# Performance work log

Measured on AMD Instinct MI355X. Metric: run time of the kernel, lower is better.

## Reference

```python
import jax, jax.numpy as jnp
import numpy as np

B, M, P, A, T = 32, 128, 20, 32, 32
H = 32   # embed_size / local hidden
E = 64   # local_hidden_dim = 2*H, global attention embed dim


def setup_inputs() -> dict:
    key = jax.random.key(0)
    ks = jax.random.split(key, 10)
    def w(k, shape, fan):
        return jax.random.normal(k, shape, jnp.float32) / np.float32(np.sqrt(fan))
    z = lambda *s: jnp.zeros(s, jnp.float32)
    o = lambda *s: jnp.ones(s, jnp.float32)
    return {
        "map_states": jax.random.normal(ks[0], (B, M, P, 16), jnp.float32),
        "agent_states": jax.random.normal(ks[1], (B, A, T, 4), jnp.float32),
        "m_W1": w(ks[2], (16, H), 16), "m_b1": z(H), "m_g1": o(H), "m_be1": z(H),
        "m_W2": w(ks[3], (H, H), H),   "m_b2": z(H), "m_g2": o(H), "m_be2": z(H),
        "a_W1": w(ks[4], (4, H), 4),   "a_b1": z(H), "a_g1": o(H), "a_be1": z(H),
        "a_W2": w(ks[5], (H, H), H),   "a_b2": z(H), "a_g2": o(H), "a_be2": z(H),
        # stacked attention params: index 0 = a2m, 1 = agent(self), 2 = m2a
        "att_Wq": w(ks[6], (3, E, E), E), "att_bq": z(3, E),
        "att_Wk": w(ks[7], (3, E, E), E), "att_bk": z(3, E),
        "att_Wv": w(ks[8], (3, E, E), E), "att_bv": z(3, E),
        "att_Wo": w(ks[9], (3, E, E), E), "att_bo": z(3, E),
    }


def _mlp(x, W, b, g, be):
    # Linear -> LayerNorm -> ReLU
    h = x @ W + b
    mu = jnp.mean(h, axis=-1, keepdims=True)
    var = jnp.var(h, axis=-1, keepdims=True)
    h = (h - mu) / jnp.sqrt(var + 1e-5) * g + be
    return jax.nn.relu(h)


def _local_graph(x, p1, p2):
    # x: [B, N, P, F] -> [B, N, 2H]
    e = _mlp(_mlp(x, *p1), *p2)                       # [B,N,P,H]
    n = e.shape[2]
    # faithful "max excluding self": max_j (e[j] - 10000*[j==i])
    mask = -10000.0 * jnp.eye(n, dtype=e.dtype)       # [Pi,Pj]
    nb = jnp.max(e[:, :, None, :, :] + mask[None, None, :, :, None], axis=3)  # [B,N,P,H]
    e = jnp.concatenate([e, nb], axis=-1)             # [B,N,P,2H]
    return jnp.max(e, axis=2)                          # [B,N,2H]


def _mha(q, k, v, Wq, bq, Wk, bk, Wv, bv, Wo, bo):
    # single-head attention, batch_first
    d = q.shape[-1]
    Q = q @ Wq + bq
    K = k @ Wk + bk
    V = v @ Wv + bv
    scores = jnp.einsum('bqd,bkd->bqk', Q, K) / jnp.sqrt(jnp.asarray(d, Q.dtype))
    attn = jax.nn.softmax(scores, axis=-1)
    return jnp.einsum('bqk,bkd->bqd', attn, V) @ Wo + bo


def reference(map_states, agent_states,
              m_W1, m_b1, m_g1, m_be1, m_W2, m_b2, m_g2, m_be2,
              a_W1, a_b1, a_g1, a_be1, a_W2, a_b2, a_g2, a_be2,
              att_Wq, att_bq, att_Wk, att_bk, att_Wv, att_bv, att_Wo, att_bo):
    map_emb = _local_graph(map_states, (m_W1, m_b1, m_g1, m_be1), (m_W2, m_b2, m_g2, m_be2))      # [B,M,E]
    agent_emb = _local_graph(agent_states, (a_W1, a_b1, a_g1, a_be1), (a_W2, a_b2, a_g2, a_be2))  # [B,A,E]

    target = agent_emb[:, :1]                                       # [B,1,E]
    kv = jnp.concatenate([target, map_emb], axis=1)                 # [B,M+1,E]
    a2m = _mha(map_emb, kv, kv, att_Wq[0], att_bq[0], att_Wk[0], att_bk[0],
               att_Wv[0], att_bv[0], att_Wo[0], att_bo[0])
    map_emb = map_emb + a2m
    t_a = _mha(target, target, target, att_Wq[1], att_bq[1], att_Wk[1], att_bk[1],
               att_Wv[1], att_bv[1], att_Wo[1], att_bo[1])
    t_m2a = _mha(target, map_emb, map_emb, att_Wq[2], att_bq[2], att_Wk[2], att_bk[2],
                 att_Wv[2], att_bv[2], att_Wo[2], att_bo[2])
    target = t_a + t_m2a                                            # [B,1,E]
    # pack (target_agent_embedding, map_embedding) into one array [B, M+1, E]
    return jnp.concatenate([target, map_emb], axis=1)
```

## Files before the change

### kernel.cpp

```cpp
#include <hip/hip_runtime.h>

#define BB 32
#define MM 128
#define PP 20
#define AA 32
#define TT 32
#define HH 32
#define EE 64

__device__ __forceinline__ float4 matvec64(const float* __restrict__ W,
                                           const float* __restrict__ xrow,
                                           int s, int t)
{
    const float4* __restrict__ Wv = (const float4*)W;
    const float4* __restrict__ xv = (const float4*)xrow;
    float4 acc = make_float4(0.f, 0.f, 0.f, 0.f);
#pragma unroll
    for (int ii = 0; ii < 4; ++ii) {
        const float4 xx = xv[s * 4 + ii];
        const int ib = s * 16 + ii * 4;
        const float4 w0 = Wv[(ib + 0) * 16 + t];
        const float4 w1 = Wv[(ib + 1) * 16 + t];
        const float4 w2 = Wv[(ib + 2) * 16 + t];
        const float4 w3 = Wv[(ib + 3) * 16 + t];
        acc.x = fmaf(xx.x, w0.x, acc.x); acc.y = fmaf(xx.x, w0.y, acc.y);
        acc.z = fmaf(xx.x, w0.z, acc.z); acc.w = fmaf(xx.x, w0.w, acc.w);
        acc.x = fmaf(xx.y, w1.x, acc.x); acc.y = fmaf(xx.y, w1.y, acc.y);
        acc.z = fmaf(xx.y, w1.z, acc.z); acc.w = fmaf(xx.y, w1.w, acc.w);
        acc.x = fmaf(xx.z, w2.x, acc.x); acc.y = fmaf(xx.z, w2.y, acc.y);
        acc.z = fmaf(xx.z, w2.z, acc.z); acc.w = fmaf(xx.z, w2.w, acc.w);
        acc.x = fmaf(xx.w, w3.x, acc.x); acc.y = fmaf(xx.w, w3.y, acc.y);
        acc.z = fmaf(xx.w, w3.z, acc.z); acc.w = fmaf(xx.w, w3.w, acc.w);
    }
    acc.x += __shfl_xor(acc.x, 16); acc.y += __shfl_xor(acc.y, 16);
    acc.z += __shfl_xor(acc.z, 16); acc.w += __shfl_xor(acc.w, 16);
    acc.x += __shfl_xor(acc.x, 32); acc.y += __shfl_xor(acc.y, 32);
    acc.z += __shfl_xor(acc.z, 32); acc.w += __shfl_xor(acc.w, 32);
    return acc;
}

template <int IN>
__device__ __forceinline__ void lg_qkv_body(const float* __restrict__ xg, int P,
                                            const float* __restrict__ W1, const float* __restrict__ b1,
                                            const float* __restrict__ g1, const float* __restrict__ be1,
                                            const float* __restrict__ W2, const float* __restrict__ b2,
                                            const float* __restrict__ g2, const float* __restrict__ be2,
                                            float* __restrict__ embRow,
                                            const float* __restrict__ Wq, const float* __restrict__ bq,
                                            const float* __restrict__ Wk, const float* __restrict__ bk,
                                            const float* __restrict__ Wv, const float* __restrict__ bv,
                                            float* __restrict__ Qrow,
                                            float* __restrict__ Krow,
                                            float* __restrict__ Vrow)
{
    const int tid  = threadIdx.x;
    const int wave = tid >> 6;
    const int lane = tid & 63;
    const int sub  = tid >> 5;
    const int c    = tid & 31;

    __shared__ __align__(16) float aslot[4][32];
    __shared__ __align__(16) float wmax[2][32];
    __shared__ __align__(16) float xrow[EE];

    float w1c[IN];
#pragma unroll
    for (int k = 0; k < IN; ++k) w1c[k] = W1[k * HH + c];
    float w2c[HH];
#pragma unroll
    for (int k = 0; k < HH; ++k) w2c[k] = W2[k * HH + c];
    const float b1c = b1[c], g1c = g1[c], be1c = be1[c];
    const float b2c = b2[c], g2c = g2[c], be2c = be2[c];

    float cmax = -1e30f;

    for (int p0 = 0; p0 < P; p0 += 4) {
        const int p = p0 + sub;
        const float* xp = xg + (long)p * IN;

        float h = b1c;
        if (IN == 16) {
            const float4* xp4 = (const float4*)xp;
            const float4 x0 = xp4[0], x1 = xp4[1], x2 = xp4[2], x3 = xp4[3];
            h = fmaf(x0.x, w1c[0], h);  h = fmaf(x0.y, w1c[1], h);
            h = fmaf(x0.z, w1c[2], h);  h = fmaf(x0.w, w1c[3], h);
            h = fmaf(x1.x, w1c[4], h);  h = fmaf(x1.y, w1c[5], h);
            h = fmaf(x1.z, w1c[6], h);  h = fmaf(x1.w, w1c[7], h);
            h = fmaf(x2.x, w1c[8], h);  h = fmaf(x2.y, w1c[9], h);
            h = fmaf(x2.z, w1c[10], h); h = fmaf(x2.w, w1c[11], h);
            h = fmaf(x3.x, w1c[12], h); h = fmaf(x3.y, w1c[13], h);
            h = fmaf(x3.z, w1c[14], h); h = fmaf(x3.w, w1c[15], h);
        } else {
            const float4 x0 = *(const float4*)xp;
            h = fmaf(x0.x, w1c[0], h); h = fmaf(x0.y, w1c[1], h);
            h = fmaf(x0.z, w1c[2], h); h = fmaf(x0.w, w1c[3], h);
        }

        float sdot = h;
#pragma unroll
        for (int off = 16; off >= 1; off >>= 1) sdot += __shfl_xor(sdot, off, 32);
        const float mu = sdot * (1.0f / 32.0f);
        float d = h - mu;
        float sq = d * d;
#pragma unroll
        for (int off = 16; off >= 1; off >>= 1) sq += __shfl_xor(sq, off, 32);
        const float var = sq * (1.0f / 32.0f);
        float a = d * rsqrtf(var + 1e-5f) * g1c + be1c;
        a = fmaxf(a, 0.0f);

        aslot[sub][c] = a;
        const float4* av4 = (const float4*)aslot[sub];
        float h2 = b2c;
#pragma unroll
        for (int j = 0; j < 8; ++j) {
            const float4 aa = av4[j];
            h2 = fmaf(aa.x, w2c[4 * j + 0], h2);
            h2 = fmaf(aa.y, w2c[4 * j + 1], h2);
            h2 = fmaf(aa.z, w2c[4 * j + 2], h2);
            h2 = fmaf(aa.w, w2c[4 * j + 3], h2);
        }

        float s2 = h2;
#pragma unroll
        for (int off = 16; off >= 1; off >>= 1) s2 += __shfl_xor(s2, off, 32);
        const float mu2 = s2 * (1.0f / 32.0f);
        float d2 = h2 - mu2;
        float sq2 = d2 * d2;
#pragma unroll
        for (int off = 16; off >= 1; off >>= 1) sq2 += __shfl_xor(sq2, off, 32);
        const float var2 = sq2 * (1.0f / 32.0f);
        float e = d2 * rsqrtf(var2 + 1e-5f) * g2c + be2c;
        e = fmaxf(e, 0.0f);

        cmax = fmaxf(cmax, e);
    }

    cmax = fmaxf(cmax, __shfl_xor(cmax, 32));
    if (lane < 32) wmax[wave][lane] = cmax;
    __syncthreads();

    if (tid < 32) {
        const float fin = fmaxf(wmax[0][tid], wmax[1][tid]);
        xrow[tid]      = fin;
        xrow[tid + 32] = fin;
        embRow[tid]      = fin;
        embRow[tid + 32] = fin;
    }
    __syncthreads();

    const int s = lane >> 4, t = lane & 15;
    if (wave == 0) {
        if (Qrow) {
            float4 q4 = matvec64(Wq, xrow, s, t);
            if (s == 0) {
                const float4 bq4 = ((const float4*)bq)[t];
                float4 qo;
                qo.x = (q4.x + bq4.x) * 0.125f;
                qo.y = (q4.y + bq4.y) * 0.125f;
                qo.z = (q4.z + bq4.z) * 0.125f;
                qo.w = (q4.w + bq4.w) * 0.125f;
                ((float4*)Qrow)[t] = qo;
            }
        }
        float4 k4 = matvec64(Wk, xrow, s, t);
        if (s == 0) {
            const float4 kb4 = ((const float4*)bk)[t];
            float4 ko;
            ko.x = k4.x + kb4.x; ko.y = k4.y + kb4.y;
            ko.z = k4.z + kb4.z; ko.w = k4.w + kb4.w;
            ((float4*)Krow)[t] = ko;
        }
    } else {
        float4 v4 = matvec64(Wv, xrow, s, t);
        if (s == 0) {
            const float4 vb4 = ((const float4*)bv)[t];
            float4 vo;
            vo.x = v4.x + vb4.x; vo.y = v4.y + vb4.y;
            vo.z = v4.z + vb4.z; vo.w = v4.w + vb4.w;
            ((float4*)Vrow)[t] = vo;
        }
    }
}

__global__ void lg_qkv_kernel(const float* __restrict__ map_states,
                              const float* __restrict__ agent_states,
                              const float* __restrict__ mW1, const float* __restrict__ mb1,
                              const float* __restrict__ mg1, const float* __restrict__ mbe1,
                              const float* __restrict__ mW2, const float* __restrict__ mb2,
                              const float* __restrict__ mg2, const float* __restrict__ mbe2,
                              const float* __restrict__ aW1, const float* __restrict__ ab1,
                              const float* __restrict__ ag1, const float* __restrict__ abe1,
                              const float* __restrict__ aW2, const float* __restrict__ ab2,
                              const float* __restrict__ ag2, const float* __restrict__ abe2,
                              const float* __restrict__ Wq, const float* __restrict__ bq,
                              const float* __restrict__ Wk, const float* __restrict__ bk,
                              const float* __restrict__ Wv, const float* __restrict__ bv,
                              float* __restrict__ map_emb,
                              float* __restrict__ target,
                              float* __restrict__ Qb,
                              float* __restrict__ Kb,
                              float* __restrict__ Vb)
{
    const int g = blockIdx.x;
    if (g < BB * MM) {
        const int b = g >> 7, m = g & 127;
        lg_qkv_body<16>(map_states + (long)g * PP * 16, PP,
                        mW1, mb1, mg1, mbe1, mW2, mb2, mg2, mbe2,
                        map_emb + (long)g * EE,
                        Wq, bq, Wk, bk, Wv, bv,
                        Qb + (long)g * EE,
                        Kb + ((long)b * 129 + 1 + m) * EE,
                        Vb + ((long)b * 129 + 1 + m) * EE);
    } else {
        const int b = g - BB * MM;
        lg_qkv_body<4>(agent_states + (long)b * AA * TT * 4, TT,
                       aW1, ab1, ag1, abe1, aW2, ab2, ag2, abe2,
                       target + (long)b * EE,
                       Wq, bq, Wk, bk, Wv, bv,
                       nullptr,
                       Kb + (long)b * 129 * EE,
                       Vb + (long)b * 129 * EE);
    }
}

__global__ void attn_fused_kernel(const float* __restrict__ map_emb,
                                  const float* __restrict__ Qb,
                                  const float* __restrict__ Kb,
                                  const float* __restrict__ Vb,
                                  const float* __restrict__ Wo, const float* __restrict__ bo,
                                  const float* __restrict__ Wk2, const float* __restrict__ bk2,
                                  const float* __restrict__ Wv2, const float* __restrict__ bv2,
                                  float* __restrict__ K2,
                                  float* __restrict__ V2,
                                  float* __restrict__ out)
{
    const int blk  = blockIdx.x;
    const int b    = blk >> 7;
    const int q    = blk & 127;
    const int lane = threadIdx.x;
    const int s = lane >> 4, t = lane & 15;

    __shared__ __align__(16) float sc[132];
    __shared__ __align__(16) float av[EE];
    __shared__ __align__(16) float resrow[EE];

    const float4 q4 = ((const float4*)(Qb + ((long)b * MM + q) * EE))[t];

    const float* Kbase = Kb + (long)b * 129 * EE;
    float mx = -1e30f;
#pragma unroll 4
    for (int it = 0; it < 33; ++it) {
        const int j = it * 4 + s;
        const bool valid = (j < 129);
        float p = 0.0f;
        if (valid) {
            const float4 k4 = ((const float4*)(Kbase + (long)j * EE))[t];
            p = q4.x * k4.x + q4.y * k4.y + q4.z * k4.z + q4.w * k4.w;
        }
        p += __shfl_xor(p, 1); p += __shfl_xor(p, 2);
        p += __shfl_xor(p, 4); p += __shfl_xor(p, 8);
        if (valid) {
            mx = fmaxf(mx, p);
            if (t == 0) sc[j] = p;
        }
    }
#pragma unroll
    for (int off = 32; off >= 1; off >>= 1) mx = fmaxf(mx, __shfl_xor(mx, off));
    __syncthreads();

    float sum = 0.0f;
    for (int j = lane; j < 129; j += 64) {
        const float e = __expf(sc[j] - mx);
        sc[j] = e;
        sum += e;
    }
#pragma unroll
    for (int off = 32; off >= 1; off >>= 1) sum += __shfl_xor(sum, off);
    const float inv = 1.0f / sum;
    __syncthreads();

    const float* Vbase = Vb + (long)b * 129 * EE;
    float a0 = 0.f, a1 = 0.f, a2 = 0.f, a3 = 0.f;
#pragma unroll 4
    for (int j0 = 0; j0 < 128; j0 += 4) {
        const float4 s4 = *(const float4*)&sc[j0];
        a0 = fmaf(s4.x, Vbase[(long)(j0 + 0) * EE + lane], a0);
        a1 = fmaf(s4.y, Vbase[(long)(j0 + 1) * EE + lane], a1);
        a2 = fmaf(s4.z, Vbase[(long)(j0 + 2) * EE + lane], a2);
        a3 = fmaf(s4.w, Vbase[(long)(j0 + 3) * EE + lane], a3);
    }
    a0 = fmaf(sc[128], Vbase[(long)128 * EE + lane], a0);
    const float acc = ((a0 + a1) + (a2 + a3)) * inv;
    av[lane] = acc;
    __syncthreads();

    const float4 o4 = matvec64(Wo, av, s, t);
    const float4 bo4 = ((const float4*)bo)[t];
    const float4 x4 = ((const float4*)(map_emb + ((long)b * MM + q) * EE))[t];
    float4 res;
    res.x = o4.x + bo4.x + x4.x;
    res.y = o4.y + bo4.y + x4.y;
    res.z = o4.z + bo4.z + x4.z;
    res.w = o4.w + bo4.w + x4.w;
    if (s == 0) {
        ((float4*)(out + ((long)b * 129 + 1 + q) * EE))[t] = res;
        ((float4*)resrow)[t] = res;
    }
    __syncthreads();

    const float4 k4 = matvec64(Wk2, resrow, s, t);
    const float4 v4 = matvec64(Wv2, resrow, s, t);
    if (s == 0) {
        const float4 kb4 = ((const float4*)bk2)[t];
        const float4 vb4 = ((const float4*)bv2)[t];
        float4 ko, vo;
        ko.x = k4.x + kb4.x; ko.y = k4.y + kb4.y; ko.z = k4.z + kb4.z; ko.w = k4.w + kb4.w;
        vo.x = v4.x + vb4.x; vo.y = v4.y + vb4.y; vo.z = v4.z + vb4.z; vo.w = v4.w + vb4.w;
        ((float4*)(K2 + ((long)b * MM + q) * EE))[t] = ko;
        ((float4*)(V2 + ((long)b * MM + q) * EE))[t] = vo;
    }
}

__global__ void target_kernel(const float* __restrict__ target,
                              const float* __restrict__ K2, const float* __restrict__ V2,
                              const float* __restrict__ Wq2, const float* __restrict__ bq2,
                              const float* __restrict__ Wo2, const float* __restrict__ bo2,
                              const float* __restrict__ Wv1, const float* __restrict__ bv1,
                              const float* __restrict__ Wo1, const float* __restrict__ bo1,
                              float* __restrict__ out)
{
    const int b    = blockIdx.x;
    const int lane = threadIdx.x;
    const int s = lane >> 4, t = lane & 15;

    __shared__ __align__(16) float trow[EE];
    __shared__ __align__(16) float tmp[EE];
    __shared__ __align__(16) float sc[128];
    __shared__ __align__(16) float av[EE];

    trow[lane] = target[(long)b * EE + lane];
    __syncthreads();

    const float4 v1 = matvec64(Wv1, trow, s, t);
    if (s == 0) {
        const float4 bv4 = ((const float4*)bv1)[t];
        float4 w; w.x = v1.x + bv4.x; w.y = v1.y + bv4.y; w.z = v1.z + bv4.z; w.w = v1.w + bv4.w;
        ((float4*)tmp)[t] = w;
    }
    __syncthreads();
    float4 ta = matvec64(Wo1, tmp, s, t);
    {
        const float4 bo4 = ((const float4*)bo1)[t];
        ta.x += bo4.x; ta.y += bo4.y; ta.z += bo4.z; ta.w += bo4.w;
    }

    float4 q4 = matvec64(Wq2, trow, s, t);
    {
        const float4 bq4 = ((const float4*)bq2)[t];
        q4.x = (q4.x + bq4.x) * 0.125f;
        q4.y = (q4.y + bq4.y) * 0.125f;
        q4.z = (q4.z + bq4.z) * 0.125f;
        q4.w = (q4.w + bq4.w) * 0.125f;
    }

    const float* Kbase = K2 + (long)b * MM * EE;
    float mx = -1e30f;
#pragma unroll 4
    for (int it = 0; it < 32; ++it) {
        const int j = it * 4 + s;
        const float4 k4 = ((const float4*)(Kbase + (long)j * EE))[t];
        float p = q4.x * k4.x + q4.y * k4.y + q4.z * k4.z + q4.w * k4.w;
        p += __shfl_xor(p, 1); p += __shfl_xor(p, 2);
        p += __shfl_xor(p, 4); p += __shfl_xor(p, 8);
        mx = fmaxf(mx, p);
        if (t == 0) sc[j] = p;
    }
#pragma unroll
    for (int off = 32; off >= 1; off >>= 1) mx = fmaxf(mx, __shfl_xor(mx, off));
    __syncthreads();

    float sum = 0.0f;
#pragma unroll
    for (int j = lane; j < MM; j += 64) {
        const float e = __expf(sc[j] - mx);
        sc[j] = e;
        sum += e;
    }
#pragma unroll
    for (int off = 32; off >= 1; off >>= 1) sum += __shfl_xor(sum, off);
    const float inv = 1.0f / sum;
    __syncthreads();

    const float* Vbase = V2 + (long)b * MM * EE;
    float a0 = 0.f, a1 = 0.f, a2 = 0.f, a3 = 0.f;
#pragma unroll 4
    for (int j0 = 0; j0 < 128; j0 += 4) {
        const float4 s4 = *(const float4*)&sc[j0];
        a0 = fmaf(s4.x, Vbase[(long)(j0 + 0) * EE + lane], a0);
        a1 = fmaf(s4.y, Vbase[(long)(j0 + 1) * EE + lane], a1);
        a2 = fmaf(s4.z, Vbase[(long)(j0 + 2) * EE + lane], a2);
        a3 = fmaf(s4.w, Vbase[(long)(j0 + 3) * EE + lane], a3);
    }
    av[lane] = ((a0 + a1) + (a2 + a3)) * inv;
    __syncthreads();

    const float4 o4 = matvec64(Wo2, av, s, t);
    if (s == 0) {
        const float4 bo4 = ((const float4*)bo2)[t];
        float4 r;
        r.x = ta.x + o4.x + bo4.x;
        r.y = ta.y + o4.y + bo4.y;
        r.z = ta.z + o4.z + bo4.z;
        r.w = ta.w + o4.w + bo4.w;
        ((float4*)(out + (long)b * 129 * EE))[t] = r;
    }
}

extern "C" void kernel_launch(void* const* d_in, const int* in_sizes, int n_in,
                              void* d_out, int out_size, void* d_ws, size_t ws_size,
                              hipStream_t stream)
{
    const float* map_states   = (const float*)d_in[0];
    const float* agent_states = (const float*)d_in[1];
    const float* m_W1 = (const float*)d_in[2];
    const float* m_b1 = (const float*)d_in[3];
    const float* m_g1 = (const float*)d_in[4];
    const float* m_be1 = (const float*)d_in[5];
    const float* m_W2 = (const float*)d_in[6];
    const float* m_b2 = (const float*)d_in[7];
    const float* m_g2 = (const float*)d_in[8];
    const float* m_be2 = (const float*)d_in[9];
    const float* a_W1 = (const float*)d_in[10];
    const float* a_b1 = (const float*)d_in[11];
    const float* a_g1 = (const float*)d_in[12];
    const float* a_be1 = (const float*)d_in[13];
    const float* a_W2 = (const float*)d_in[14];
    const float* a_b2 = (const float*)d_in[15];
    const float* a_g2 = (const float*)d_in[16];
    const float* a_be2 = (const float*)d_in[17];
    const float* att_Wq = (const float*)d_in[18];
    const float* att_bq = (const float*)d_in[19];
    const float* att_Wk = (const float*)d_in[20];
    const float* att_bk = (const float*)d_in[21];
    const float* att_Wv = (const float*)d_in[22];
    const float* att_bv = (const float*)d_in[23];
    const float* att_Wo = (const float*)d_in[24];
    const float* att_bo = (const float*)d_in[25];

    float* out = (float*)d_out;

    float* ws      = (float*)d_ws;
    float* map_emb = ws;
    float* target  = map_emb + BB * MM * EE;
    float* Qb      = target + BB * EE;
    float* Kb      = Qb + BB * MM * EE;
    float* Vb      = Kb + BB * 129 * EE;
    float* K2      = Vb + BB * 129 * EE;
    float* V2      = K2 + BB * MM * EE;

    const float* Wq0 = att_Wq + 0 * EE * EE; const float* bq0 = att_bq + 0 * EE;
    const float* Wk0 = att_Wk + 0 * EE * EE; const float* bk0 = att_bk + 0 * EE;
    const float* Wv0 = att_Wv + 0 * EE * EE; const float* bv0 = att_bv + 0 * EE;
    const float* Wo0 = att_Wo + 0 * EE * EE; const float* bo0 = att_bo + 0 * EE;
    const float* Wv1 = att_Wv + 1 * EE * EE; const float* bv1 = att_bv + 1 * EE;
    const float* Wo1 = att_Wo + 1 * EE * EE; const float* bo1 = att_bo + 1 * EE;
    const float* Wq2 = att_Wq + 2 * EE * EE; const float* bq2 = att_bq + 2 * EE;
    const float* Wk2 = att_Wk + 2 * EE * EE; const float* bk2 = att_bk + 2 * EE;
    const float* Wv2 = att_Wv + 2 * EE * EE; const float* bv2 = att_bv + 2 * EE;
    const float* Wo2 = att_Wo + 2 * EE * EE; const float* bo2 = att_bo + 2 * EE;

    hipLaunchKernelGGL(lg_qkv_kernel, dim3(BB * MM + BB), dim3(128), 0, stream,
                       map_states, agent_states,
                       m_W1, m_b1, m_g1, m_be1, m_W2, m_b2, m_g2, m_be2,
                       a_W1, a_b1, a_g1, a_be1, a_W2, a_b2, a_g2, a_be2,
                       Wq0, bq0, Wk0, bk0, Wv0, bv0,
                       map_emb, target, Qb, Kb, Vb);

    hipLaunchKernelGGL(attn_fused_kernel, dim3(BB * MM), dim3(64), 0, stream,
                       map_emb, Qb, Kb, Vb, Wo0, bo0,
                       Wk2, bk2, Wv2, bv2, K2, V2, out);

    hipLaunchKernelGGL(target_kernel, dim3(BB), dim3(64), 0, stream,
                       target, K2, V2, Wq2, bq2, Wo2, bo2, Wv1, bv1, Wo1, bo1, out);
}
```

Baseline: 184.2 us.

## Fuse target attention into attn kernel via last-block atomic counter; vectorize PV loop

```diff
diff --git a/kernel.cpp b/kernel.cpp
--- a/kernel.cpp
+++ b/kernel.cpp
@@ -199,9 +199,11 @@
                               float* __restrict__ target,
                               float* __restrict__ Qb,
                               float* __restrict__ Kb,
-                              float* __restrict__ Vb)
+                              float* __restrict__ Vb,
+                              int* __restrict__ cnt)
 {
     const int g = blockIdx.x;
+    if (g < BB && threadIdx.x == 0) cnt[g] = 0;
     if (g < BB * MM) {
         const int b = g >> 7, m = g & 127;
         lg_qkv_body<16>(map_states + (long)g * PP * 16, PP,
@@ -227,11 +229,17 @@
                                   const float* __restrict__ Qb,
                                   const float* __restrict__ Kb,
                                   const float* __restrict__ Vb,
+                                  const float* __restrict__ target,
                                   const float* __restrict__ Wo, const float* __restrict__ bo,
                                   const float* __restrict__ Wk2, const float* __restrict__ bk2,
                                   const float* __restrict__ Wv2, const float* __restrict__ bv2,
+                                  const float* __restrict__ Wq2, const float* __restrict__ bq2,
+                                  const float* __restrict__ Wo2, const float* __restrict__ bo2,
+                                  const float* __restrict__ Wv1, const float* __restrict__ bv1,
+                                  const float* __restrict__ Wo1, const float* __restrict__ bo1,
                                   float* __restrict__ K2,
                                   float* __restrict__ V2,
+                                  int*   __restrict__ cnt,
                                   float* __restrict__ out)
 {
     const int blk  = blockIdx.x;
@@ -243,6 +251,7 @@
     __shared__ __align__(16) float sc[132];
     __shared__ __align__(16) float av[EE];
     __shared__ __align__(16) float resrow[EE];
+    __shared__ __align__(16) float tmp[EE];
 
     const float4 q4 = ((const float4*)(Qb + ((long)b * MM + q) * EE))[t];
 
@@ -280,18 +289,25 @@
     __syncthreads();
 
     const float* Vbase = Vb + (long)b * 129 * EE;
-    float a0 = 0.f, a1 = 0.f, a2 = 0.f, a3 = 0.f;
+    float4 a4 = make_float4(0.f, 0.f, 0.f, 0.f);
 #pragma unroll 4
-    for (int j0 = 0; j0 < 128; j0 += 4) {
-        const float4 s4 = *(const float4*)&sc[j0];
-        a0 = fmaf(s4.x, Vbase[(long)(j0 + 0) * EE + lane], a0);
-        a1 = fmaf(s4.y, Vbase[(long)(j0 + 1) * EE + lane], a1);
-        a2 = fmaf(s4.z, Vbase[(long)(j0 + 2) * EE + lane], a2);
-        a3 = fmaf(s4.w, Vbase[(long)(j0 + 3) * EE + lane], a3);
-    }
-    a0 = fmaf(sc[128], Vbase[(long)128 * EE + lane], a0);
-    const float acc = ((a0 + a1) + (a2 + a3)) * inv;
-    av[lane] = acc;
+    for (int it = 0; it < 33; ++it) {
+        const int j = it * 4 + s;
+        if (j < 129) {
+            const float w = sc[j];
+            const float4 v4 = ((const float4*)(Vbase + (long)j * EE))[t];
+            a4.x = fmaf(w, v4.x, a4.x); a4.y = fmaf(w, v4.y, a4.y);
+            a4.z = fmaf(w, v4.z, a4.z); a4.w = fmaf(w, v4.w, a4.w);
+        }
+    }
+    a4.x += __shfl_xor(a4.x, 16); a4.y += __shfl_xor(a4.y, 16);
+    a4.z += __shfl_xor(a4.z, 16); a4.w += __shfl_xor(a4.w, 16);
+    a4.x += __shfl_xor(a4.x, 32); a4.y += __shfl_xor(a4.y, 32);
+    a4.z += __shfl_xor(a4.z, 32); a4.w += __shfl_xor(a4.w, 32);
+    if (s == 0) {
+        float4 o; o.x = a4.x * inv; o.y = a4.y * inv; o.z = a4.z * inv; o.w = a4.w * inv;
+        ((float4*)av)[t] = o;
+    }
     __syncthreads();
 
     const float4 o4 = matvec64(Wo, av, s, t);
@@ -319,25 +335,15 @@
         ((float4*)(K2 + ((long)b * MM + q) * EE))[t] = ko;
         ((float4*)(V2 + ((long)b * MM + q) * EE))[t] = vo;
     }
-}
-
-__global__ void target_kernel(const float* __restrict__ target,
-                              const float* __restrict__ K2, const float* __restrict__ V2,
-                              const float* __restrict__ Wq2, const float* __restrict__ bq2,
-                              const float* __restrict__ Wo2, const float* __restrict__ bo2,
-                              const float* __restrict__ Wv1, const float* __restrict__ bv1,
-                              const float* __restrict__ Wo1, const float* __restrict__ bo1,
-                              float* __restrict__ out)
-{
-    const int b    = blockIdx.x;
-    const int lane = threadIdx.x;
-    const int s = lane >> 4, t = lane & 15;
-
-    __shared__ __align__(16) float trow[EE];
-    __shared__ __align__(16) float tmp[EE];
-    __shared__ __align__(16) float sc[128];
-    __shared__ __align__(16) float av[EE];
-
+
+    __threadfence();
+    int old = 0;
+    if (lane == 0) old = atomicAdd(&cnt[b], 1);
+    old = __shfl(old, 0);
+    if (old != MM - 1) return;
+    __threadfence();
+
+    float* trow = resrow;
     trow[lane] = target[(long)b * EE + lane];
     __syncthreads();
 
@@ -350,68 +356,75 @@
     __syncthreads();
     float4 ta = matvec64(Wo1, tmp, s, t);
     {
-        const float4 bo4 = ((const float4*)bo1)[t];
-        ta.x += bo4.x; ta.y += bo4.y; ta.z += bo4.z; ta.w += bo4.w;
-    }
-
-    float4 q4 = matvec64(Wq2, trow, s, t);
+        const float4 bo14 = ((const float4*)bo1)[t];
+        ta.x += bo14.x; ta.y += bo14.y; ta.z += bo14.z; ta.w += bo14.w;
+    }
+
+    float4 qt = matvec64(Wq2, trow, s, t);
     {
         const float4 bq4 = ((const float4*)bq2)[t];
-        q4.x = (q4.x + bq4.x) * 0.125f;
-        q4.y = (q4.y + bq4.y) * 0.125f;
-        q4.z = (q4.z + bq4.z) * 0.125f;
-        q4.w = (q4.w + bq4.w) * 0.125f;
-    }
-
-    const float* Kbase = K2 + (long)b * MM * EE;
-    float mx = -1e30f;
+        qt.x = (qt.x + bq4.x) * 0.125f;
+        qt.y = (qt.y + bq4.y) * 0.125f;
+        qt.z = (qt.z + bq4.z) * 0.125f;
+        qt.w = (qt.w + bq4.w) * 0.125f;
+    }
+
+    const float* K2base = K2 + (long)b * MM * EE;
+    float mx2 = -1e30f;
 #pragma unroll 4
     for (int it = 0; it < 32; ++it) {
         const int j = it * 4 + s;
-        const float4 k4 = ((const float4*)(Kbase + (long)j * EE))[t];
-        float p = q4.x * k4.x + q4.y * k4.y + q4.z * k4.z + q4.w * k4.w;
+        const float4 kk = ((const float4*)(K2base + (long)j * EE))[t];
+        float p = qt.x * kk.x + qt.y * kk.y + qt.z * kk.z + qt.w * kk.w;
         p += __shfl_xor(p, 1); p += __shfl_xor(p, 2);
         p += __shfl_xor(p, 4); p += __shfl_xor(p, 8);
-        mx = fmaxf(mx, p);
+        mx2 = fmaxf(mx2, p);
         if (t == 0) sc[j] = p;
     }
 #pragma unroll
-    for (int off = 32; off >= 1; off >>= 1) mx = fmaxf(mx, __shfl_xor(mx, off));
-    __syncthreads();
-
-    float sum = 0.0f;
+    for (int off = 32; off >= 1; off >>= 1) mx2 = fmaxf(mx2, __shfl_xor(mx2, off));
+    __syncthreads();
+
+    float sum2 = 0.0f;
 #pragma unroll
     for (int j = lane; j < MM; j += 64) {
-        const float e = __expf(sc[j] - mx);
+        const float e = __expf(sc[j] - mx2);
         sc[j] = e;
-        sum += e;
-    }
-#pragma unroll
-    for (int off = 32; off >= 1; off >>= 1) sum += __shfl_xor(sum, off);
-    const float inv = 1.0f / sum;
-    __syncthreads();
-
-    const float* Vbase = V2 + (long)b * MM * EE;
-    float a0 = 0.f, a1 = 0.f, a2 = 0.f, a3 = 0.f;
+        sum2 += e;
+    }
+#pragma unroll
+    for (int off = 32; off >= 1; off >>= 1) sum2 += __shfl_xor(sum2, off);
+    const float inv2 = 1.0f / sum2;
+    __syncthreads();
+
+    const float* V2base = V2 + (long)b * MM * EE;
+    float4 b4 = make_float4(0.f, 0.f, 0.f, 0.f);
 #pragma unroll 4
-    for (int j0 = 0; j0 < 128; j0 += 4) {
-        const float4 s4 = *(const float4*)&sc[j0];
-        a0 = fmaf(s4.x, Vbase[(long)(j0 + 0) * EE + lane], a0);
-        a1 = fmaf(s4.y, Vbase[(long)(j0 + 1) * EE + lane], a1);
-        a2 = fmaf(s4.z, Vbase[(long)(j0 + 2) * EE + lane], a2);
-        a3 = fmaf(s4.w, Vbase[(long)(j0 + 3) * EE + lane], a3);
-    }
-    av[lane] = ((a0 + a1) + (a2 + a3)) * inv;
-    __syncthreads();
-
-    const float4 o4 = matvec64(Wo2, av, s, t);
-    if (s == 0) {
-        const float4 bo4 = ((const float4*)bo2)[t];
+    for (int it = 0; it < 32; ++it) {
+        const int j = it * 4 + s;
+        const float w = sc[j];
+        const float4 vv = ((const float4*)(V2base + (long)j * EE))[t];
+        b4.x = fmaf(w, vv.x, b4.x); b4.y = fmaf(w, vv.y, b4.y);
+        b4.z = fmaf(w, vv.z, b4.z); b4.w = fmaf(w, vv.w, b4.w);
+    }
+    b4.x += __shfl_xor(b4.x, 16); b4.y += __shfl_xor(b4.y, 16);
+    b4.z += __shfl_xor(b4.z, 16); b4.w += __shfl_xor(b4.w, 16);
+    b4.x += __shfl_xor(b4.x, 32); b4.y += __shfl_xor(b4.y, 32);
+    b4.z += __shfl_xor(b4.z, 32); b4.w += __shfl_xor(b4.w, 32);
+    if (s == 0) {
+        float4 o; o.x = b4.x * inv2; o.y = b4.y * inv2; o.z = b4.z * inv2; o.w = b4.w * inv2;
+        ((float4*)av)[t] = o;
+    }
+    __syncthreads();
+
+    const float4 ot = matvec64(Wo2, av, s, t);
+    if (s == 0) {
+        const float4 bo24 = ((const float4*)bo2)[t];
         float4 r;
-        r.x = ta.x + o4.x + bo4.x;
-        r.y = ta.y + o4.y + bo4.y;
-        r.z = ta.z + o4.z + bo4.z;
-        r.w = ta.w + o4.w + bo4.w;
+        r.x = ta.x + ot.x + bo24.x;
+        r.y = ta.y + ot.y + bo24.y;
+        r.z = ta.z + ot.z + bo24.z;
+        r.w = ta.w + ot.w + bo24.w;
         ((float4*)(out + (long)b * 129 * EE))[t] = r;
     }
 }
@@ -457,6 +470,7 @@
     float* Vb      = Kb + BB * 129 * EE;
     float* K2      = Vb + BB * 129 * EE;
     float* V2      = K2 + BB * MM * EE;
+    int*   cnt     = (int*)(V2 + BB * MM * EE);
 
     const float* Wq0 = att_Wq + 0 * EE * EE; const float* bq0 = att_bq + 0 * EE;
     const float* Wk0 = att_Wk + 0 * EE * EE; const float* bk0 = att_bk + 0 * EE;
@@ -474,12 +488,10 @@
                        m_W1, m_b1, m_g1, m_be1, m_W2, m_b2, m_g2, m_be2,
                        a_W1, a_b1, a_g1, a_be1, a_W2, a_b2, a_g2, a_be2,
                        Wq0, bq0, Wk0, bk0, Wv0, bv0,
-                       map_emb, target, Qb, Kb, Vb);
+                       map_emb, target, Qb, Kb, Vb, cnt);
 
     hipLaunchKernelGGL(attn_fused_kernel, dim3(BB * MM), dim3(64), 0, stream,
-                       map_emb, Qb, Kb, Vb, Wo0, bo0,
-                       Wk2, bk2, Wv2, bv2, K2, V2, out);
-
-    hipLaunchKernelGGL(target_kernel, dim3(BB), dim3(64), 0, stream,
-                       target, K2, V2, Wq2, bq2, Wo2, bo2, Wv1, bv1, Wo1, bo1, out);
+                       map_emb, Qb, Kb, Vb, target, Wo0, bo0,
+                       Wk2, bk2, Wv2, bv2, Wq2, bq2, Wo2, bo2,
+                       Wv1, bv1, Wo1, bo1, K2, V2, cnt, out);
 }
```

New measurement: 266.4 us. 44.6% more time.
